# Optimization experiments

Hardware: AMD Instinct MI355X
Metric: run time of the kernel (lower is better)

## Reference

```python
import jax, jax.numpy as jnp
import numpy as np

KERNEL_MUL = 2.0
KERNEL_NUM = 5

def _mmd_rbf_channel(total, batch_size):
    # total: [2B, D] -> scalar MMD for one channel
    n = total.shape[0]
    sq = jnp.sum(total * total, axis=-1)  # [2B]
    # GEMM-based squared pairwise distance (avoids [2B,2B,D] intermediate)
    d2 = sq[:, None] + sq[None, :] - 2.0 * (total @ total.T)
    # bandwidth from detached distances (original uses .data)
    bandwidth = jax.lax.stop_gradient(jnp.sum(d2)) / (n * n - n)
    bandwidth = bandwidth / (KERNEL_MUL ** (KERNEL_NUM // 2))
    bws = bandwidth * (KERNEL_MUL ** jnp.arange(KERNEL_NUM, dtype=total.dtype))  # [K]
    kern = jnp.sum(jnp.exp(-d2[None, :, :] / bws[:, None, None]), axis=0)  # [2B,2B]
    B = batch_size
    XX = jnp.mean(kern[:B, :B])
    YY = jnp.mean(kern[B:, B:])
    XY = jnp.mean(kern[:B, B:])
    YX = jnp.mean(kern[B:, :B])
    return XX + YY - XY - YX

def setup_inputs() -> dict:
    key = jax.random.key(0)
    k1, k2 = jax.random.split(key)
    source = jax.random.normal(k1, (512, 32, 768), dtype=jnp.float32)
    target = jax.random.normal(k2, (512, 32, 768), dtype=jnp.float32)
    return {"source": source, "target": target}

def reference(source, target):
    B, C, D = source.shape
    # per-channel concat: [C, 2B, D]
    total = jnp.concatenate([source, target], axis=0).transpose(1, 0, 2)
    per_channel = jax.vmap(lambda t: _mmd_rbf_channel(t, B))(total)  # [C]
    return jnp.mean(per_channel)
```

## Files before the change

kernel.cpp:

```cpp
#include <hip/hip_runtime.h>
#include <stdint.h>

#define CCH 32
#define BATCH 512
#define NROW 1024
#define DDIM 768
#define TILE 128
#define NPAIRS 36
#define BK 32
#define NSTEP (DDIM / BK)

typedef unsigned short u16;
typedef __attribute__((ext_vector_type(8))) short short8v;
typedef __attribute__((ext_vector_type(4))) float f32x4;

__device__ __forceinline__ u16 f2bf_rne(float x) {
    uint32_t u = __float_as_uint(x);
    u += 0x7FFFu + ((u >> 16) & 1u);
    return (u16)(u >> 16);
}
__device__ __forceinline__ float bf2f(u16 h) {
    return __uint_as_float(((uint32_t)h) << 16);
}

__device__ __forceinline__ void gload_lds16(const u16* g, u16* l) {
    __builtin_amdgcn_global_load_lds(
        (const __attribute__((address_space(1))) unsigned int*)(g),
        (__attribute__((address_space(3))) unsigned int*)(l),
        16, 0, 0);
}

__constant__ int PI_[NPAIRS] = {0,0,0,0,0,0,0,0, 1,1,1,1,1,1,1, 2,2,2,2,2,2,
                                3,3,3,3,3, 4,4,4,4, 5,5,5, 6,6, 7};
__constant__ int PJ_[NPAIRS] = {0,1,2,3,4,5,6,7, 1,2,3,4,5,6,7, 2,3,4,5,6,7,
                                3,4,5,6,7, 4,5,6,7, 5,6,7, 6,7, 7};

__global__ __launch_bounds__(256) void k_prep(const float* __restrict__ src,
                                              const float* __restrict__ tgt,
                                              u16* __restrict__ bfbuf,
                                              float* __restrict__ sq) {
    int wid = threadIdx.x >> 6, lane = threadIdx.x & 63;
    int row = blockIdx.x * 4 + wid;
    int c = row >> 10, i = row & 1023;
    const float* rowp = (i < BATCH) ? (src + ((size_t)i * CCH + c) * DDIM)
                                    : (tgt + ((size_t)(i - BATCH) * CCH + c) * DDIM);
    u16* orow = bfbuf + (size_t)row * DDIM;
    float ss = 0.f;
#pragma unroll
    for (int j = 0; j < 3; ++j) {
        float4 v = *(reinterpret_cast<const float4*>(rowp) + lane + j * 64);
        u16 h0 = f2bf_rne(v.x), h1 = f2bf_rne(v.y), h2 = f2bf_rne(v.z), h3 = f2bf_rne(v.w);
        float f0 = bf2f(h0), f1 = bf2f(h1), f2 = bf2f(h2), f3 = bf2f(h3);
        ss += f0 * f0 + f1 * f1 + f2 * f2 + f3 * f3;
        ushort4 hv; hv.x = h0; hv.y = h1; hv.z = h2; hv.w = h3;
        *reinterpret_cast<ushort4*>(orow + (size_t)(lane + j * 64) * 4) = hv;
    }
#pragma unroll
    for (int off = 32; off > 0; off >>= 1) ss += __shfl_down(ss, off);
    if (lane == 0) sq[row] = ss;
}

__global__ __launch_bounds__(256) void k_colsum(const u16* __restrict__ bfbuf,
                                                float* __restrict__ colpart) {
    int c = blockIdx.x >> 3, ic = blockIdx.x & 7;
    const u16* base = bfbuf + ((size_t)c * NROW + (size_t)ic * 128) * DDIM;
#pragma unroll
    for (int j = 0; j < 3; ++j) {
        int d = threadIdx.x + j * 256;
        float s0 = 0.f, s1 = 0.f;
        for (int r = 0; r < 128; r += 2) {
            s0 += bf2f(base[(size_t)r * DDIM + d]);
            s1 += bf2f(base[(size_t)(r + 1) * DDIM + d]);
        }
        colpart[((size_t)c * 8 + ic) * DDIM + d] = s0 + s1;
    }
}

__global__ __launch_bounds__(256) void k_bw(const float* __restrict__ sq,
                                            const float* __restrict__ colpart,
                                            float* __restrict__ bwc) {
    int c = blockIdx.x, t = threadIdx.x;
    const float* sqc = sq + (size_t)c * NROW;
    float s = sqc[t] + sqc[t + 256] + sqc[t + 512] + sqc[t + 768];
    float s2 = 0.f;
#pragma unroll
    for (int j = 0; j < 3; ++j) {
        int d = t + j * 256;
        float cs = 0.f;
#pragma unroll
        for (int ic = 0; ic < 8; ++ic) cs += colpart[((size_t)c * 8 + ic) * DDIM + d];
        s2 += cs * cs;
    }
    __shared__ float redA[256], redB[256];
    redA[t] = s; redB[t] = s2;
    __syncthreads();
    for (int k = 128; k > 0; k >>= 1) {
        if (t < k) { redA[t] += redA[t + k]; redB[t] += redB[t + k]; }
        __syncthreads();
    }
    if (t == 0) {
        double sumd2 = 2.0 * (double)NROW * (double)redA[0] - 2.0 * (double)redB[0];
        double bw = sumd2 / ((double)NROW * (double)NROW - (double)NROW) / 4.0;
        bwc[c] = (float)(-1.4426950408889634 / (16.0 * bw));
    }
}

__global__ __launch_bounds__(256, 3) void k_mmd(const u16* __restrict__ bfbuf,
                                                const float* __restrict__ sq,
                                                const float* __restrict__ bwc,
                                                float* __restrict__ partial) {
    int orig = blockIdx.x;
    int blk = (orig & 7) * 144 + (orig >> 3);
    int c = blk / NPAIRS, p = blk - c * NPAIRS;
    int ti = PI_[p], tj = PJ_[p];
    const u16* Ab = bfbuf + ((size_t)c * NROW + (size_t)ti * TILE) * DDIM;
    const u16* Bb = bfbuf + ((size_t)c * NROW + (size_t)tj * TILE) * DDIM;

    __shared__ __align__(16) u16 lA[3][TILE * BK];
    __shared__ __align__(16) u16 lB[3][TILE * BK];

    int t = threadIdx.x;
    int wid = t >> 6, lane = t & 63;
    int lr = lane & 15, kg = lane >> 4;
    int wr = wid >> 1, wc = wid & 1;

    int g0 = t, row0 = g0 >> 2, kc0 = ((g0 & 3) ^ ((row0 >> 1) & 3)) * 8;
    int g1 = t + 256, row1 = g1 >> 2, kc1 = ((g1 & 3) ^ ((row1 >> 1) & 3)) * 8;
    const u16* gA0 = Ab + (size_t)row0 * DDIM + kc0;
    const u16* gA1 = Ab + (size_t)row1 * DDIM + kc1;
    const u16* gB0 = Bb + (size_t)row0 * DDIM + kc0;
    const u16* gB1 = Bb + (size_t)row1 * DDIM + kc1;
    u16* lba0;
    u16* lbb0;
    auto STAGE = [&](int buf, int k0) {
        gload_lds16(gA0 + k0, &lA[buf][(size_t)(wid * 64) * 8]);
        gload_lds16(gB0 + k0, &lB[buf][(size_t)(wid * 64) * 8]);
        gload_lds16(gA1 + k0, &lA[buf][(size_t)(wid * 64 + 256) * 8]);
        gload_lds16(gB1 + k0, &lB[buf][(size_t)(wid * 64 + 256) * 8]);
    };
    (void)lba0; (void)lbb0;

    f32x4 acc[4][4];
#pragma unroll
    for (int m = 0; m < 4; ++m)
#pragma unroll
        for (int n = 0; n < 4; ++n) acc[m][n] = f32x4{0.f, 0.f, 0.f, 0.f};

    int ks = (kg ^ ((lr >> 1) & 3)) * 8;
    int raddrA = (wr * 64 + lr) * BK + ks;
    int raddrB = (wc * 64 + lr) * BK + ks;

    STAGE(0, 0);
    STAGE(1, BK);

#pragma unroll
    for (int s = 0; s < NSTEP; ++s) {
        if (s < NSTEP - 1) asm volatile("s_waitcnt vmcnt(4)" ::: "memory");
        else               asm volatile("s_waitcnt vmcnt(0)" ::: "memory");
        asm volatile("s_barrier" ::: "memory");
        if (s + 2 < NSTEP) STAGE((s + 2) % 3, (s + 2) * BK);

        const int cur = s % 3;
        short8v af[4], bf[4];
#pragma unroll
        for (int m = 0; m < 4; ++m)
            af[m] = *reinterpret_cast<const short8v*>(&lA[cur][raddrA + m * 16 * BK]);
#pragma unroll
        for (int n = 0; n < 4; ++n)
            bf[n] = *reinterpret_cast<const short8v*>(&lB[cur][raddrB + n * 16 * BK]);
#pragma unroll
        for (int m = 0; m < 4; ++m)
#pragma unroll
            for (int n = 0; n < 4; ++n)
                acc[m][n] = __builtin_amdgcn_mfma_f32_16x16x32_bf16(af[m], bf[n], acc[m][n], 0, 0, 0);
    }

    float ci = bwc[c];
    const float* sqc = sq + (size_t)c * NROW;
    float sqi[4][4], sqj[4];
#pragma unroll
    for (int m = 0; m < 4; ++m) {
        float4 s4 = *reinterpret_cast<const float4*>(&sqc[ti * TILE + wr * 64 + m * 16 + kg * 4]);
        sqi[m][0] = s4.x; sqi[m][1] = s4.y; sqi[m][2] = s4.z; sqi[m][3] = s4.w;
    }
#pragma unroll
    for (int n = 0; n < 4; ++n)
        sqj[n] = sqc[tj * TILE + wc * 64 + n * 16 + lr];

    float psum = 0.f;
#pragma unroll
    for (int m = 0; m < 4; ++m)
#pragma unroll
        for (int n = 0; n < 4; ++n) {
#pragma unroll
            for (int r = 0; r < 4; ++r) {
                float d2 = sqi[m][r] + sqj[n] - 2.0f * acc[m][n][r];
                float t1 = __builtin_amdgcn_exp2f(d2 * ci);
                float t2 = t1 * t1, t4 = t2 * t2, t8 = t4 * t4, t16 = t8 * t8;
                psum += ((t1 + t2) + (t4 + t8)) + t16;
            }
        }

#pragma unroll
    for (int off = 32; off > 0; off >>= 1) psum += __shfl_down(psum, off);
    float* red = reinterpret_cast<float*>(&lA[0][0]);
    __syncthreads();
    if (lane == 0) red[wid] = psum;
    __syncthreads();
    if (t == 0) {
        float sblk = 0.f;
        for (int w = 0; w < 4; ++w) sblk += red[w];
        partial[blk] = sblk;
    }
}

__global__ __launch_bounds__(64) void k_final(const float* __restrict__ partial,
                                              float* __restrict__ out) {
    int lane = threadIdx.x;
    double r = 0.0;
    if (lane < CCH) {
        const float* pp = partial + (size_t)lane * NPAIRS;
        double s = 0.0;
        for (int q = 0; q < NPAIRS; ++q) {
            int ti = PI_[q], tj = PJ_[q];
            double w = (ti == tj) ? 1.0 : 2.0;
            double sgn = ((ti < 4) == (tj < 4)) ? 1.0 : -1.0;
            s += sgn * w * (double)pp[q];
        }
        r = s / ((double)BATCH * (double)BATCH);
    }
    for (int off = 16; off > 0; off >>= 1) r += __shfl_down(r, off);
    if (lane == 0) out[0] = (float)(r / (double)CCH);
}

extern "C" void kernel_launch(void* const* d_in, const int* in_sizes, int n_in,
                              void* d_out, int out_size, void* d_ws, size_t ws_size,
                              hipStream_t stream) {
    const float* src = (const float*)d_in[0];
    const float* tgt = (const float*)d_in[1];
    float* out = (float*)d_out;
    char* ws = (char*)d_ws;

    const size_t OFF_BF   = 0;
    const size_t OFF_SQ   = (size_t)CCH * NROW * DDIM * 2;
    const size_t OFF_CP   = OFF_SQ + (size_t)CCH * NROW * 4;
    const size_t OFF_BWC  = OFF_CP + (size_t)CCH * 8 * DDIM * 4;
    const size_t OFF_PART = OFF_BWC + (size_t)CCH * 4;

    u16*   bfbuf   = (u16*)(ws + OFF_BF);
    float* sq      = (float*)(ws + OFF_SQ);
    float* colpart = (float*)(ws + OFF_CP);
    float* bwc     = (float*)(ws + OFF_BWC);
    float* partial = (float*)(ws + OFF_PART);

    k_prep<<<CCH * NROW / 4, 256, 0, stream>>>(src, tgt, bfbuf, sq);
    k_colsum<<<CCH * 8, 256, 0, stream>>>(bfbuf, colpart);
    k_bw<<<CCH, 256, 0, stream>>>(sq, colpart, bwc);
    k_mmd<<<CCH * NPAIRS, 256, 0, stream>>>(bfbuf, sq, bwc, partial);
    k_final<<<1, 64, 0, stream>>>(partial, out);
}
```

Measured before the change: 85.43 us.

## Batch four rows per wave in prep and switch mmd to double-buffered LDS

```diff
diff --git a/kernel.cpp b/kernel.cpp
--- a/kernel.cpp
+++ b/kernel.cpp
@@ -40,24 +40,38 @@
                                               u16* __restrict__ bfbuf,
                                               float* __restrict__ sq) {
     int wid = threadIdx.x >> 6, lane = threadIdx.x & 63;
-    int row = blockIdx.x * 4 + wid;
-    int c = row >> 10, i = row & 1023;
-    const float* rowp = (i < BATCH) ? (src + ((size_t)i * CCH + c) * DDIM)
-                                    : (tgt + ((size_t)(i - BATCH) * CCH + c) * DDIM);
-    u16* orow = bfbuf + (size_t)row * DDIM;
-    float ss = 0.f;
-#pragma unroll
-    for (int j = 0; j < 3; ++j) {
-        float4 v = *(reinterpret_cast<const float4*>(rowp) + lane + j * 64);
-        u16 h0 = f2bf_rne(v.x), h1 = f2bf_rne(v.y), h2 = f2bf_rne(v.z), h3 = f2bf_rne(v.w);
-        float f0 = bf2f(h0), f1 = bf2f(h1), f2 = bf2f(h2), f3 = bf2f(h3);
-        ss += f0 * f0 + f1 * f1 + f2 * f2 + f3 * f3;
-        ushort4 hv; hv.x = h0; hv.y = h1; hv.z = h2; hv.w = h3;
-        *reinterpret_cast<ushort4*>(orow + (size_t)(lane + j * 64) * 4) = hv;
-    }
-#pragma unroll
-    for (int off = 32; off > 0; off >>= 1) ss += __shfl_down(ss, off);
-    if (lane == 0) sq[row] = ss;
+    int rbase = blockIdx.x * 16 + wid * 4;
+    const float* rp[4];
+#pragma unroll
+    for (int r = 0; r < 4; ++r) {
+        int row = rbase + r;
+        int c = row >> 10, i = row & 1023;
+        rp[r] = (i < BATCH) ? (src + ((size_t)i * CCH + c) * DDIM)
+                            : (tgt + ((size_t)(i - BATCH) * CCH + c) * DDIM);
+    }
+    float4 v[4][3];
+#pragma unroll
+    for (int r = 0; r < 4; ++r)
+#pragma unroll
+        for (int j = 0; j < 3; ++j)
+            v[r][j] = *(reinterpret_cast<const float4*>(rp[r]) + lane + j * 64);
+#pragma unroll
+    for (int r = 0; r < 4; ++r) {
+        u16* orow = bfbuf + (size_t)(rbase + r) * DDIM;
+        float ss = 0.f;
+#pragma unroll
+        for (int j = 0; j < 3; ++j) {
+            float4 w = v[r][j];
+            u16 h0 = f2bf_rne(w.x), h1 = f2bf_rne(w.y), h2 = f2bf_rne(w.z), h3 = f2bf_rne(w.w);
+            float f0 = bf2f(h0), f1 = bf2f(h1), f2 = bf2f(h2), f3 = bf2f(h3);
+            ss += f0 * f0 + f1 * f1 + f2 * f2 + f3 * f3;
+            ushort4 hv; hv.x = h0; hv.y = h1; hv.z = h2; hv.w = h3;
+            *reinterpret_cast<ushort4*>(orow + (size_t)(lane + j * 64) * 4) = hv;
+        }
+#pragma unroll
+        for (int off = 32; off > 0; off >>= 1) ss += __shfl_down(ss, off);
+        if (lane == 0) sq[rbase + r] = ss;
+    }
 }
 
 __global__ __launch_bounds__(256) void k_colsum(const u16* __restrict__ bfbuf,
@@ -105,7 +119,7 @@
     }
 }
 
-__global__ __launch_bounds__(256, 3) void k_mmd(const u16* __restrict__ bfbuf,
+__global__ __launch_bounds__(256, 5) void k_mmd(const u16* __restrict__ bfbuf,
                                                 const float* __restrict__ sq,
                                                 const float* __restrict__ bwc,
                                                 float* __restrict__ partial) {
@@ -116,8 +130,8 @@
     const u16* Ab = bfbuf + ((size_t)c * NROW + (size_t)ti * TILE) * DDIM;
     const u16* Bb = bfbuf + ((size_t)c * NROW + (size_t)tj * TILE) * DDIM;
 
-    __shared__ __align__(16) u16 lA[3][TILE * BK];
-    __shared__ __align__(16) u16 lB[3][TILE * BK];
+    __shared__ __align__(16) u16 lA[2][TILE * BK];
+    __shared__ __align__(16) u16 lB[2][TILE * BK];
 
     int t = threadIdx.x;
     int wid = t >> 6, lane = t & 63;
@@ -130,15 +144,13 @@
     const u16* gA1 = Ab + (size_t)row1 * DDIM + kc1;
     const u16* gB0 = Bb + (size_t)row0 * DDIM + kc0;
     const u16* gB1 = Bb + (size_t)row1 * DDIM + kc1;
-    u16* lba0;
-    u16* lbb0;
+
     auto STAGE = [&](int buf, int k0) {
         gload_lds16(gA0 + k0, &lA[buf][(size_t)(wid * 64) * 8]);
         gload_lds16(gB0 + k0, &lB[buf][(size_t)(wid * 64) * 8]);
         gload_lds16(gA1 + k0, &lA[buf][(size_t)(wid * 64 + 256) * 8]);
         gload_lds16(gB1 + k0, &lB[buf][(size_t)(wid * 64 + 256) * 8]);
     };
-    (void)lba0; (void)lbb0;
 
     f32x4 acc[4][4];
 #pragma unroll
@@ -151,16 +163,18 @@
     int raddrB = (wc * 64 + lr) * BK + ks;
 
     STAGE(0, 0);
-    STAGE(1, BK);
 
 #pragma unroll
     for (int s = 0; s < NSTEP; ++s) {
-        if (s < NSTEP - 1) asm volatile("s_waitcnt vmcnt(4)" ::: "memory");
-        else               asm volatile("s_waitcnt vmcnt(0)" ::: "memory");
+        if (s + 1 < NSTEP) {
+            STAGE((s + 1) & 1, (s + 1) * BK);
+            asm volatile("s_waitcnt vmcnt(4)" ::: "memory");
+        } else {
+            asm volatile("s_waitcnt vmcnt(0)" ::: "memory");
+        }
         asm volatile("s_barrier" ::: "memory");
-        if (s + 2 < NSTEP) STAGE((s + 2) % 3, (s + 2) * BK);
-
-        const int cur = s % 3;
+
+        const int cur = s & 1;
         short8v af[4], bf[4];
 #pragma unroll
         for (int m = 0; m < 4; ++m)
@@ -173,6 +187,8 @@
 #pragma unroll
             for (int n = 0; n < 4; ++n)
                 acc[m][n] = __builtin_amdgcn_mfma_f32_16x16x32_bf16(af[m], bf[n], acc[m][n], 0, 0, 0);
+
+        asm volatile("s_barrier" ::: "memory");
     }
 
     float ci = bwc[c];
@@ -208,8 +224,7 @@
     if (lane == 0) red[wid] = psum;
     __syncthreads();
     if (t == 0) {
-        float sblk = 0.f;
-        for (int w = 0; w < 4; ++w) sblk += red[w];
+        float sblk = red[0] + red[1] + red[2] + red[3];
         partial[blk] = sblk;
     }
 }
@@ -253,7 +268,7 @@
     float* bwc     = (float*)(ws + OFF_BWC);
     float* partial = (float*)(ws + OFF_PART);
 
-    k_prep<<<CCH * NROW / 4, 256, 0, stream>>>(src, tgt, bfbuf, sq);
+    k_prep<<<CCH * NROW / 16, 256, 0, stream>>>(src, tgt, bfbuf, sq);
     k_colsum<<<CCH * 8, 256, 0, stream>>>(bfbuf, colpart);
     k_bw<<<CCH, 256, 0, stream>>>(sq, colpart, bwc);
     k_mmd<<<CCH * NPAIRS, 256, 0, stream>>>(bfbuf, sq, bwc, partial);
```

New measurement: 104.6 us. 1.22x slower.
